# Optimization experiments

Measured on AMD Instinct MI355X. Metric: run time of the kernel, lower is better.

The kernel has to match this reference:

```python
import jax, jax.numpy as jnp
import numpy as np

B, N, C, H = 2, 2048, 512, 8
D = C // H  # head dim = 64
SCALE = C ** -0.5  # module uses heads_channels**-0.5 (full inner dim, not per-head)


def setup_inputs() -> dict:
    key = jax.random.key(0)
    ks = jax.random.split(key, 9)
    return {
        "q": jax.random.normal(ks[0], (B, N, C), jnp.float32),
        "kv": jax.random.normal(ks[1], (B, N, C), jnp.float32),
        "pos_q": jax.random.normal(ks[2], (B, N, D), jnp.float32),
        "pos_k": jax.random.normal(ks[3], (B, N, D), jnp.float32),
        "Wq": jax.random.normal(ks[4], (C, C), jnp.float32) * (C ** -0.5),
        "Wk": jax.random.normal(ks[5], (C, C), jnp.float32) * (C ** -0.5),
        "Wv": jax.random.normal(ks[6], (C, C), jnp.float32) * (C ** -0.5),
        "Wo": jax.random.normal(ks[7], (C, C), jnp.float32) * (C ** -0.5),
        "bo": jnp.zeros((C,), jnp.float32),
    }


def reference(q, kv, pos_q, pos_k, Wq, Wk, Wv, Wo, bo):
    # projections: [b n c] @ [c c] -> [b n c]
    qp = q @ Wq
    kp = kv @ Wk
    vp = kv @ Wv
    # split heads: b n (h d) -> b h n d
    split = lambda t: t.reshape(B, N, H, D).transpose(0, 2, 1, 3)
    qh, kh, vh = split(qp), split(kp), split(vp)
    # additive positional bias, broadcast over heads: b n d -> b 1 n d
    qh = qh + pos_q[:, None, :, :]
    kh = kh + pos_k[:, None, :, :]
    sim = jnp.einsum("bhid,bhjd->bhij", qh, kh) * SCALE
    attn = jax.nn.softmax(sim, axis=-1)
    out = jnp.einsum("bhij,bhjd->bhid", attn, vh)
    # merge heads: b h n d -> b n (h d)
    out = out.transpose(0, 2, 1, 3).reshape(B, N, C)
    return out @ Wo + bo
```

## Files before the change

### kernel.cpp

```cpp
#include <hip/hip_runtime.h>
#include <hip/hip_bf16.h>
#include <stdint.h>
#include <math.h>

static constexpr int kB = 2, kN = 2048, kC = 512, kH = 8, kD = 64;
static constexpr float kScaleL2E =
    (float)(0.044194173824159216 * 1.4426950408889634);
static constexpr float kShift = 12.0f;
static constexpr int kSplit = 4;
static constexpr size_t kSegF = (size_t)kB * kN * kC;

typedef short bf16x8 __attribute__((ext_vector_type(8)));
typedef short bf16x4 __attribute__((ext_vector_type(4)));
typedef float f32x4  __attribute__((ext_vector_type(4)));

__device__ __forceinline__ float bf2f(unsigned short u) {
  union { unsigned int i; float f; } v; v.i = ((unsigned int)u) << 16; return v.f;
}
__device__ __forceinline__ unsigned short f2bf(float f) {
  union { float f; unsigned int i; } v; v.f = f;
  unsigned int x = v.i;
  return (unsigned short)((x + 0x7FFFu + ((x >> 16) & 1u)) >> 16);
}
__device__ __forceinline__ short f2bs(float f) { return (short)f2bf(f); }
__device__ __forceinline__ unsigned int pack2_t(float lo, float hi) {
  union { float f; unsigned int i; } a, b; a.f = lo; b.f = hi;
  return (b.i & 0xFFFF0000u) | (a.i >> 16);
}

__global__ __launch_bounds__(256) void prep_kernel(
    const float* __restrict__ q, const float* __restrict__ kv,
    const float* __restrict__ Wq, const float* __restrict__ Wk,
    const float* __restrict__ Wv,
    unsigned short* __restrict__ qbf, unsigned short* __restrict__ kvbf,
    unsigned short* __restrict__ wT)
{
  const int t = threadIdx.x;
  if (blockIdx.z == 0) {
    const int gid = blockIdx.x * 256 + t;
    #pragma unroll
    for (int it = 0; it < 8; ++it) {
      int i4 = gid + it * 65536;
      float4 a = *(const float4*)(q + (size_t)i4 * 4);
      float4 b = *(const float4*)(kv + (size_t)i4 * 4);
      bf16x4 ab = {f2bs(a.x), f2bs(a.y), f2bs(a.z), f2bs(a.w)};
      bf16x4 bb = {f2bs(b.x), f2bs(b.y), f2bs(b.z), f2bs(b.w)};
      *(bf16x4*)(qbf + (size_t)i4 * 4) = ab;
      *(bf16x4*)(kvbf + (size_t)i4 * 4) = bb;
    }
  } else {
    if (blockIdx.x >= 192) return;
    const int wsel = blockIdx.x >> 6;
    const int tile = blockIdx.x & 63;
    const int tr = tile >> 3, tc = tile & 7;
    const float* W = (wsel == 0) ? Wq : (wsel == 1 ? Wk : Wv);
    unsigned short* out = wT + (size_t)wsel * kC * kC;

    __shared__ __align__(16) float Ts[64][68];
    #pragma unroll
    for (int it = 0; it < 4; ++it) {
      int e = t + it * 256;
      int r = e >> 4, c4 = (e & 15) * 4;
      *(float4*)&Ts[r][c4] =
          *(const float4*)(W + (size_t)(tr * 64 + r) * kC + tc * 64 + c4);
    }
    __syncthreads();
    const int n = t >> 2, ks = (t & 3) * 16;
    unsigned short* orow = out + (size_t)(tc * 64 + n) * kC + tr * 64 + ks;
    #pragma unroll
    for (int c = 0; c < 4; ++c) {
      ushort4 o;
      o.x = f2bf(Ts[ks + c * 4 + 0][n]);
      o.y = f2bf(Ts[ks + c * 4 + 1][n]);
      o.z = f2bf(Ts[ks + c * 4 + 2][n]);
      o.w = f2bf(Ts[ks + c * 4 + 3][n]);
      *(ushort4*)(orow + c * 4) = o;
    }
  }
}

__global__ __launch_bounds__(256) void proj_kernel(
    const unsigned short* __restrict__ qbf,
    const unsigned short* __restrict__ kvbf,
    const unsigned short* __restrict__ wT,
    const float* __restrict__ pos_q,
    const float* __restrict__ pos_k,
    unsigned short* __restrict__ qh,
    unsigned short* __restrict__ kh,
    unsigned short* __restrict__ vhT)
{
  const bool kvmode = (blockIdx.z == 1);
  const unsigned short* A = kvmode ? kvbf : qbf;
  const unsigned short* Bt0 = wT + (kvmode ? (size_t)kC * kC : 0);
  const unsigned short* Bt1 = wT + 2 * (size_t)kC * kC;

  __shared__ __align__(16) unsigned short As[128][72];
  __shared__ __align__(16) unsigned short Bs[2][64][72];

  const int t = threadIdx.x;
  const int w = t >> 6, lane = t & 63;
  const int l15 = lane & 15, quad = lane >> 4;
  const int m0 = blockIdx.x * 128;
  const int n0 = blockIdx.y * 64;

  const int sr = t >> 3, sc = (t & 7) * 8;

  bf16x8 pa[4], pb0[2], pb1[2];
  #pragma unroll
  for (int i = 0; i < 4; ++i)
    pa[i] = *(const bf16x8*)(A + (size_t)(m0 + sr + i * 32) * kC + sc);
  #pragma unroll
  for (int i = 0; i < 2; ++i)
    pb0[i] = *(const bf16x8*)(Bt0 + (size_t)(n0 + sr + i * 32) * kC + sc);
  if (kvmode)
    #pragma unroll
    for (int i = 0; i < 2; ++i)
      pb1[i] = *(const bf16x8*)(Bt1 + (size_t)(n0 + sr + i * 32) * kC + sc);

  f32x4 acc0[2][4], acc1[2][4];
  #pragma unroll
  for (int si = 0; si < 2; ++si)
    #pragma unroll
    for (int ct = 0; ct < 4; ++ct) {
      acc0[si][ct] = (f32x4){0.f, 0.f, 0.f, 0.f};
      acc1[si][ct] = (f32x4){0.f, 0.f, 0.f, 0.f};
    }

  for (int k0 = 0; k0 < kC; k0 += 64) {
    if (k0) __syncthreads();
    #pragma unroll
    for (int i = 0; i < 4; ++i) *(bf16x8*)&As[sr + i * 32][sc] = pa[i];
    #pragma unroll
    for (int i = 0; i < 2; ++i) *(bf16x8*)&Bs[0][sr + i * 32][sc] = pb0[i];
    if (kvmode)
      #pragma unroll
      for (int i = 0; i < 2; ++i) *(bf16x8*)&Bs[1][sr + i * 32][sc] = pb1[i];
    __syncthreads();
    if (k0 + 64 < kC) {
      int kn = k0 + 64;
      #pragma unroll
      for (int i = 0; i < 4; ++i)
        pa[i] = *(const bf16x8*)(A + (size_t)(m0 + sr + i * 32) * kC + kn + sc);
      #pragma unroll
      for (int i = 0; i < 2; ++i)
        pb0[i] = *(const bf16x8*)(Bt0 + (size_t)(n0 + sr + i * 32) * kC + kn + sc);
      if (kvmode)
        #pragma unroll
        for (int i = 0; i < 2; ++i)
          pb1[i] = *(const bf16x8*)(Bt1 + (size_t)(n0 + sr + i * 32) * kC + kn + sc);
    }
    bf16x8 a0[2], a1[2];
    #pragma unroll
    for (int si = 0; si < 2; ++si) {
      a0[si] = *(const bf16x8*)&As[w * 32 + si * 16 + l15][quad * 8];
      a1[si] = *(const bf16x8*)&As[w * 32 + si * 16 + l15][32 + quad * 8];
    }
    #pragma unroll
    for (int ct = 0; ct < 4; ++ct) {
      bf16x8 b0 = *(const bf16x8*)&Bs[0][ct * 16 + l15][quad * 8];
      bf16x8 b1 = *(const bf16x8*)&Bs[0][ct * 16 + l15][32 + quad * 8];
      #pragma unroll
      for (int si = 0; si < 2; ++si) {
        acc0[si][ct] = __builtin_amdgcn_mfma_f32_16x16x32_bf16(a0[si], b0, acc0[si][ct], 0, 0, 0);
        acc0[si][ct] = __builtin_amdgcn_mfma_f32_16x16x32_bf16(a1[si], b1, acc0[si][ct], 0, 0, 0);
      }
      if (kvmode) {
        bf16x8 c0 = *(const bf16x8*)&Bs[1][ct * 16 + l15][quad * 8];
        bf16x8 c1 = *(const bf16x8*)&Bs[1][ct * 16 + l15][32 + quad * 8];
        #pragma unroll
        for (int si = 0; si < 2; ++si) {
          acc1[si][ct] = __builtin_amdgcn_mfma_f32_16x16x32_bf16(a0[si], c0, acc1[si][ct], 0, 0, 0);
          acc1[si][ct] = __builtin_amdgcn_mfma_f32_16x16x32_bf16(a1[si], c1, acc1[si][ct], 0, 0, 0);
        }
      }
    }
  }

  const int h = n0 >> 6;
  #pragma unroll
  for (int si = 0; si < 2; ++si)
    #pragma unroll
    for (int r = 0; r < 4; ++r) {
      int m = m0 + w * 32 + si * 16 + quad * 4 + r;
      int b = m >> 11, n_seq = m & (kN - 1);
      #pragma unroll
      for (int ct = 0; ct < 4; ++ct) {
        int d = ct * 16 + l15;
        if (!kvmode) {
          float val = (acc0[si][ct][r] +
                       pos_q[((size_t)b * kN + n_seq) * kD + d]) * kScaleL2E;
          qh[(((size_t)b * kH + h) * kN + n_seq) * kD + d] = f2bf(val);
        } else {
          float vk = acc0[si][ct][r] + pos_k[((size_t)b * kN + n_seq) * kD + d];
          kh[(((size_t)b * kH + h) * kN + n_seq) * kD + d] = f2bf(vk);
          vhT[(((size_t)b * kH + h) * kD + d) * kN + n_seq] = f2bf(acc1[si][ct][r]);
        }
      }
    }
}

__global__ __launch_bounds__(256, 4) void attn_kernel(
    const unsigned short* __restrict__ qh,
    const unsigned short* __restrict__ kh,
    const unsigned short* __restrict__ vhT,
    unsigned short* __restrict__ opart,
    float* __restrict__ lbuf)
{
  const int bh = blockIdx.y;
  const int b = bh >> 3, h = bh & 7;
  const int q0 = blockIdx.x * 128;
  const int s = blockIdx.z;
  const int kbase = s * (kN / kSplit);
  const int nkt = kN / kSplit / 64;
  const int t = threadIdx.x;
  const int w = t >> 6, lane = t & 63;
  const int l15 = lane & 15, quad = lane >> 4;

  __shared__ __align__(16) unsigned short Kbf[2][64][72];
  __shared__ __align__(16) unsigned short Vt[2][64][72];

  const unsigned short* Qb = qh  + (size_t)bh * kN * kD;
  const unsigned short* Kb = kh  + (size_t)bh * kN * kD;
  const unsigned short* Vb = vhT + (size_t)bh * kD * kN;

  bf16x8 aq[2][2];
  #pragma unroll
  for (int g = 0; g < 2; ++g) {
    const unsigned short* qrow = Qb + (size_t)(q0 + w * 32 + g * 16 + l15) * kD;
    aq[g][0] = *(const bf16x8*)(qrow + quad * 8);
    aq[g][1] = *(const bf16x8*)(qrow + 32 + quad * 8);
  }

  const int sr = t >> 3, sc = (t & 7) * 8, sr2 = sr + 32;

  bf16x8 pk0 = *(const bf16x8*)(Kb + (size_t)(kbase + sr) * kD + sc);
  bf16x8 pk1 = *(const bf16x8*)(Kb + (size_t)(kbase + sr2) * kD + sc);
  bf16x8 pv0 = *(const bf16x8*)(Vb + (size_t)sr * kN + kbase + sc);
  bf16x8 pv1 = *(const bf16x8*)(Vb + (size_t)sr2 * kN + kbase + sc);
  *(bf16x8*)&Kbf[0][sr][sc]  = pk0;
  *(bf16x8*)&Kbf[0][sr2][sc] = pk1;
  *(bf16x8*)&Vt[0][sr][sc]   = pv0;
  *(bf16x8*)&Vt[0][sr2][sc]  = pv1;
  {
    int kt1 = kbase + 64;
    pk0 = *(const bf16x8*)(Kb + (size_t)(kt1 + sr) * kD + sc);
    pk1 = *(const bf16x8*)(Kb + (size_t)(kt1 + sr2) * kD + sc);
    pv0 = *(const bf16x8*)(Vb + (size_t)sr * kN + kt1 + sc);
    pv1 = *(const bf16x8*)(Vb + (size_t)sr2 * kN + kt1 + sc);
  }

  f32x4 o[2][4];
  #pragma unroll
  for (int g = 0; g < 2; ++g)
    #pragma unroll
    for (int nt = 0; nt < 4; ++nt) o[g][nt] = (f32x4){0.f, 0.f, 0.f, 0.f};
  float l_run[2] = {0.f, 0.f};

  const int src_a = l15 + 32 * (quad & 1);
  const int src_b = src_a + 16;
  const bool hi_sel = (quad & 2) != 0;

  for (int i = 0; i < nkt; ++i) {
    __syncthreads();
    if (i + 1 < nkt) {
      unsigned short (*Kw)[72] = Kbf[(i + 1) & 1];
      unsigned short (*Vw)[72] = Vt[(i + 1) & 1];
      *(bf16x8*)&Kw[sr][sc]  = pk0;
      *(bf16x8*)&Kw[sr2][sc] = pk1;
      *(bf16x8*)&Vw[sr][sc]  = pv0;
      *(bf16x8*)&Vw[sr2][sc] = pv1;
      if (i + 2 < nkt) {
        int ktn = kbase + (i + 2) * 64;
        pk0 = *(const bf16x8*)(Kb + (size_t)(ktn + sr) * kD + sc);
        pk1 = *(const bf16x8*)(Kb + (size_t)(ktn + sr2) * kD + sc);
        pv0 = *(const bf16x8*)(Vb + (size_t)sr * kN + ktn + sc);
        pv1 = *(const bf16x8*)(Vb + (size_t)sr2 * kN + ktn + sc);
      }
    }
    const unsigned short (*Kr)[72] = Kbf[i & 1];
    const unsigned short (*Vr)[72] = Vt[i & 1];

    f32x4 sacc[2][4];
    #pragma unroll
    for (int ct = 0; ct < 4; ++ct) {
      bf16x8 ak0 = *(const bf16x8*)&Kr[ct * 16 + l15][quad * 8];
      bf16x8 ak1 = *(const bf16x8*)&Kr[ct * 16 + l15][32 + quad * 8];
      #pragma unroll
      for (int g = 0; g < 2; ++g) {
        f32x4 zz = (f32x4){0.f, 0.f, 0.f, 0.f};
        zz = __builtin_amdgcn_mfma_f32_16x16x32_bf16(ak0, aq[g][0], zz, 0, 0, 0);
        zz = __builtin_amdgcn_mfma_f32_16x16x32_bf16(ak1, aq[g][1], zz, 0, 0, 0);
        sacc[g][ct] = zz;
      }
    }

    union PF { unsigned int u[4]; bf16x8 v; } pf[2][2];
    #pragma unroll
    for (int g = 0; g < 2; ++g) {
      float psum = 0.f;
      #pragma unroll
      for (int ct = 0; ct < 4; ++ct)
        #pragma unroll
        for (int r = 0; r < 4; ++r) {
          float p = exp2f(sacc[g][ct][r] - kShift);
          sacc[g][ct][r] = p;
          psum += p;
        }
      psum += __shfl_xor(psum, 16);
      psum += __shfl_xor(psum, 32);
      l_run[g] += psum;

      unsigned int pk01[4], pk23[4];
      #pragma unroll
      for (int ct = 0; ct < 4; ++ct) {
        pk01[ct] = pack2_t(sacc[g][ct][0], sacc[g][ct][1]);
        pk23[ct] = pack2_t(sacc[g][ct][2], sacc[g][ct][3]);
      }
      unsigned int s01a[4], s23a[4], s01b[4], s23b[4];
      #pragma unroll
      for (int ct = 0; ct < 4; ++ct) {
        s01a[ct] = (unsigned int)__shfl((int)pk01[ct], src_a);
        s23a[ct] = (unsigned int)__shfl((int)pk23[ct], src_a);
        s01b[ct] = (unsigned int)__shfl((int)pk01[ct], src_b);
        s23b[ct] = (unsigned int)__shfl((int)pk23[ct], src_b);
      }
      pf[g][0].u[0] = hi_sel ? s01a[1] : s01a[0];
      pf[g][0].u[1] = hi_sel ? s23a[1] : s23a[0];
      pf[g][0].u[2] = hi_sel ? s01b[1] : s01b[0];
      pf[g][0].u[3] = hi_sel ? s23b[1] : s23b[0];
      pf[g][1].u[0] = hi_sel ? s01a[3] : s01a[2];
      pf[g][1].u[1] = hi_sel ? s23a[3] : s23a[2];
      pf[g][1].u[2] = hi_sel ? s01b[3] : s01b[2];
      pf[g][1].u[3] = hi_sel ? s23b[3] : s23b[2];
    }

    #pragma unroll
    for (int nt = 0; nt < 4; ++nt) {
      bf16x8 av0 = *(const bf16x8*)&Vr[nt * 16 + l15][quad * 8];
      bf16x8 av1 = *(const bf16x8*)&Vr[nt * 16 + l15][32 + quad * 8];
      #pragma unroll
      for (int g = 0; g < 2; ++g) {
        o[g][nt] = __builtin_amdgcn_mfma_f32_16x16x32_bf16(av0, pf[g][0].v, o[g][nt], 0, 0, 0);
        o[g][nt] = __builtin_amdgcn_mfma_f32_16x16x32_bf16(av1, pf[g][1].v, o[g][nt], 0, 0, 0);
      }
    }
  }

  unsigned short* od = opart + (size_t)s * kSegF;
  #pragma unroll
  for (int g = 0; g < 2; ++g) {
    const int n = q0 + w * 32 + g * 16 + l15;
    unsigned short* obase = od + ((size_t)b * kN + n) * kC + h * kD + quad * 4;
    #pragma unroll
    for (int nt = 0; nt < 4; ++nt) {
      ushort4 st;
      st.x = f2bf(o[g][nt][0]);
      st.y = f2bf(o[g][nt][1]);
      st.z = f2bf(o[g][nt][2]);
      st.w = f2bf(o[g][nt][3]);
      *(ushort4*)(obase + nt * 16) = st;
    }
    if (quad == 0) lbuf[(size_t)(s * 16 + bh) * kN + n] = l_run[g];
  }
}

__global__ __launch_bounds__(256) void combine_kernel(
    const unsigned short* __restrict__ opart,
    const float* __restrict__ lbuf,
    unsigned short* __restrict__ ao)
{
  const size_t f = ((size_t)blockIdx.x * 256 + threadIdx.x) * 8;
  const int c = (int)(f & (kC - 1));
  const int n = (int)((f >> 9) & (kN - 1));
  const int b = (int)(f >> 20);
  const int bh = b * 8 + (c >> 6);
  float lsum = 0.f;
  #pragma unroll
  for (int s = 0; s < kSplit; ++s)
    lsum += lbuf[(size_t)(s * 16 + bh) * kN + n];
  float wgt = 1.f / lsum;
  float acc[8] = {};
  #pragma unroll
  for (int s = 0; s < kSplit; ++s) {
    bf16x8 v = *(const bf16x8*)(opart + (size_t)s * kSegF + f);
    #pragma unroll
    for (int j = 0; j < 8; ++j) acc[j] += bf2f((unsigned short)v[j]);
  }
  bf16x8 r;
  #pragma unroll
  for (int j = 0; j < 8; ++j) r[j] = (short)f2bf(acc[j] * wgt);
  *(bf16x8*)(ao + f) = r;
}

__global__ __launch_bounds__(256) void proj_out_kernel(
    const unsigned short* __restrict__ ao,
    const float* __restrict__ Wo,
    const float* __restrict__ bo,
    float* __restrict__ out)
{
  __shared__ __align__(16) unsigned short Wt[64][72];

  const int t = threadIdx.x;
  const int w = t >> 6, lane = t & 63;
  const int l15 = lane & 15, quad = lane >> 4;
  const int m0 = blockIdx.x * 64;
  const int n0 = blockIdx.y * 64;

  const unsigned short* arow = ao + (size_t)(m0 + w * 16 + l15) * kC;

  ushort4 pw[4];
  #pragma unroll
  for (int i = 0; i < 4; ++i) {
    int e = t + i * 256;
    int r = e >> 4, c4 = (e & 15) * 4;
    float4 wv = *(const float4*)(Wo + (size_t)r * kC + n0 + c4);
    pw[i] = make_ushort4(f2bf(wv.x), f2bf(wv.y), f2bf(wv.z), f2bf(wv.w));
  }
  bf16x8 pa0 = *(const bf16x8*)(arow + quad * 8);
  bf16x8 pa1 = *(const bf16x8*)(arow + 32 + quad * 8);

  f32x4 acc[4];
  #pragma unroll
  for (int ct = 0; ct < 4; ++ct) acc[ct] = (f32x4){0.f, 0.f, 0.f, 0.f};

  for (int k0 = 0; k0 < kC; k0 += 64) {
    if (k0) __syncthreads();
    #pragma unroll
    for (int i = 0; i < 4; ++i) {
      int e = t + i * 256;
      int r = e >> 4, c4 = (e & 15) * 4;
      Wt[c4 + 0][r] = pw[i].x;
      Wt[c4 + 1][r] = pw[i].y;
      Wt[c4 + 2][r] = pw[i].z;
      Wt[c4 + 3][r] = pw[i].w;
    }
    __syncthreads();
    bf16x8 a0 = pa0, a1 = pa1;
    if (k0 + 64 < kC) {
      int kn = k0 + 64;
      #pragma unroll
      for (int i = 0; i < 4; ++i) {
        int e = t + i * 256;
        int r = e >> 4, c4 = (e & 15) * 4;
        float4 wv = *(const float4*)(Wo + (size_t)(kn + r) * kC + n0 + c4);
        pw[i] = make_ushort4(f2bf(wv.x), f2bf(wv.y), f2bf(wv.z), f2bf(wv.w));
      }
      pa0 = *(const bf16x8*)(arow + kn + quad * 8);
      pa1 = *(const bf16x8*)(arow + kn + 32 + quad * 8);
    }
    #pragma unroll
    for (int ct = 0; ct < 4; ++ct) {
      bf16x8 b0 = *(const bf16x8*)&Wt[ct * 16 + l15][quad * 8];
      bf16x8 b1 = *(const bf16x8*)&Wt[ct * 16 + l15][32 + quad * 8];
      acc[ct] = __builtin_amdgcn_mfma_f32_16x16x32_bf16(a0, b0, acc[ct], 0, 0, 0);
      acc[ct] = __builtin_amdgcn_mfma_f32_16x16x32_bf16(a1, b1, acc[ct], 0, 0, 0);
    }
  }

  #pragma unroll
  for (int ct = 0; ct < 4; ++ct) {
    int n = n0 + ct * 16 + l15;
    float bb = bo[n];
    #pragma unroll
    for (int r = 0; r < 4; ++r) {
      int m = m0 + w * 16 + quad * 4 + r;
      out[(size_t)m * kC + n] = acc[ct][r] + bb;
    }
  }
}

extern "C" void kernel_launch(void* const* d_in, const int* in_sizes, int n_in,
                              void* d_out, int out_size, void* d_ws, size_t ws_size,
                              hipStream_t stream) {
  (void)in_sizes; (void)n_in; (void)out_size; (void)ws_size;
  const float* q     = (const float*)d_in[0];
  const float* kv    = (const float*)d_in[1];
  const float* pos_q = (const float*)d_in[2];
  const float* pos_k = (const float*)d_in[3];
  const float* Wq    = (const float*)d_in[4];
  const float* Wk    = (const float*)d_in[5];
  const float* Wv    = (const float*)d_in[6];
  const float* Wo    = (const float*)d_in[7];
  const float* bo    = (const float*)d_in[8];
  float* out = (float*)d_out;

  const size_t seg = (size_t)kB * kH * kN * kD;

  unsigned short* qbf  = (unsigned short*)d_ws;
  unsigned short* kvbf = qbf + seg;
  unsigned short* wT   = kvbf + seg;
  unsigned short* qhp  = wT + 3 * (size_t)kC * kC;
  unsigned short* khp  = qhp + seg;
  unsigned short* vtp  = khp + seg;
  unsigned short* opart = vtp + seg;
  float* lbuf = (float*)(opart + (size_t)kSplit * kSegF);
  unsigned short* aop = (unsigned short*)(lbuf + (size_t)kSplit * 16 * kN);

  dim3 blk(256);
  prep_kernel<<<dim3(256, 1, 2), blk, 0, stream>>>(q, kv, Wq, Wk, Wv, qbf, kvbf, wT);
  proj_kernel<<<dim3(32, 8, 2), blk, 0, stream>>>(qbf, kvbf, wT, pos_q, pos_k,
                                                  qhp, khp, vtp);
  attn_kernel<<<dim3(16, 16, kSplit), blk, 0, stream>>>(qhp, khp, vtp, opart, lbuf);
  combine_kernel<<<dim3(1024), blk, 0, stream>>>(opart, lbuf, aop);
  proj_out_kernel<<<dim3(64, 8), blk, 0, stream>>>(aop, Wo, bo, out);
}
```

Before: 163.7 us.

## Fuse fp32-to-bf16 conversion and weight transpose into projection GEMM

Removes the separate prep kernel that converted q/kv to bf16 and wrote transposed bf16 weights. The projection kernel now loads fp32 activations and weights directly, converts them while staging into shared memory, and transposes the weights with scalar LDS stores. This saves a launch and a round trip of the intermediate bf16 buffers. In exchange it drops the register prefetch pipelining, reads twice as many bytes per tile, repeats the conversion in every block, and adds scattered 2-byte LDS stores that may conflict on banks.

```diff
diff --git a/kernel.cpp b/kernel.cpp
--- a/kernel.cpp
+++ b/kernel.cpp
@@ -28,61 +28,12 @@
   return (b.i & 0xFFFF0000u) | (a.i >> 16);
 }
 
-__global__ __launch_bounds__(256) void prep_kernel(
-    const float* __restrict__ q, const float* __restrict__ kv,
-    const float* __restrict__ Wq, const float* __restrict__ Wk,
+__global__ __launch_bounds__(256) void proj_kernel(
+    const float* __restrict__ q,
+    const float* __restrict__ kv,
+    const float* __restrict__ Wq,
+    const float* __restrict__ Wk,
     const float* __restrict__ Wv,
-    unsigned short* __restrict__ qbf, unsigned short* __restrict__ kvbf,
-    unsigned short* __restrict__ wT)
-{
-  const int t = threadIdx.x;
-  if (blockIdx.z == 0) {
-    const int gid = blockIdx.x * 256 + t;
-    #pragma unroll
-    for (int it = 0; it < 8; ++it) {
-      int i4 = gid + it * 65536;
-      float4 a = *(const float4*)(q + (size_t)i4 * 4);
-      float4 b = *(const float4*)(kv + (size_t)i4 * 4);
-      bf16x4 ab = {f2bs(a.x), f2bs(a.y), f2bs(a.z), f2bs(a.w)};
-      bf16x4 bb = {f2bs(b.x), f2bs(b.y), f2bs(b.z), f2bs(b.w)};
-      *(bf16x4*)(qbf + (size_t)i4 * 4) = ab;
-      *(bf16x4*)(kvbf + (size_t)i4 * 4) = bb;
-    }
-  } else {
-    if (blockIdx.x >= 192) return;
-    const int wsel = blockIdx.x >> 6;
-    const int tile = blockIdx.x & 63;
-    const int tr = tile >> 3, tc = tile & 7;
-    const float* W = (wsel == 0) ? Wq : (wsel == 1 ? Wk : Wv);
-    unsigned short* out = wT + (size_t)wsel * kC * kC;
-
-    __shared__ __align__(16) float Ts[64][68];
-    #pragma unroll
-    for (int it = 0; it < 4; ++it) {
-      int e = t + it * 256;
-      int r = e >> 4, c4 = (e & 15) * 4;
-      *(float4*)&Ts[r][c4] =
-          *(const float4*)(W + (size_t)(tr * 64 + r) * kC + tc * 64 + c4);
-    }
-    __syncthreads();
-    const int n = t >> 2, ks = (t & 3) * 16;
-    unsigned short* orow = out + (size_t)(tc * 64 + n) * kC + tr * 64 + ks;
-    #pragma unroll
-    for (int c = 0; c < 4; ++c) {
-      ushort4 o;
-      o.x = f2bf(Ts[ks + c * 4 + 0][n]);
-      o.y = f2bf(Ts[ks + c * 4 + 1][n]);
-      o.z = f2bf(Ts[ks + c * 4 + 2][n]);
-      o.w = f2bf(Ts[ks + c * 4 + 3][n]);
-      *(ushort4*)(orow + c * 4) = o;
-    }
-  }
-}
-
-__global__ __launch_bounds__(256) void proj_kernel(
-    const unsigned short* __restrict__ qbf,
-    const unsigned short* __restrict__ kvbf,
-    const unsigned short* __restrict__ wT,
     const float* __restrict__ pos_q,
     const float* __restrict__ pos_k,
     unsigned short* __restrict__ qh,
@@ -90,9 +41,9 @@
     unsigned short* __restrict__ vhT)
 {
   const bool kvmode = (blockIdx.z == 1);
-  const unsigned short* A = kvmode ? kvbf : qbf;
-  const unsigned short* Bt0 = wT + (kvmode ? (size_t)kC * kC : 0);
-  const unsigned short* Bt1 = wT + 2 * (size_t)kC * kC;
+  const float* A  = kvmode ? kv : q;
+  const float* W0 = kvmode ? Wk : Wq;
+  const float* W1 = Wv;
 
   __shared__ __align__(16) unsigned short As[128][72];
   __shared__ __align__(16) unsigned short Bs[2][64][72];
@@ -103,20 +54,6 @@
   const int m0 = blockIdx.x * 128;
   const int n0 = blockIdx.y * 64;
 
-  const int sr = t >> 3, sc = (t & 7) * 8;
-
-  bf16x8 pa[4], pb0[2], pb1[2];
-  #pragma unroll
-  for (int i = 0; i < 4; ++i)
-    pa[i] = *(const bf16x8*)(A + (size_t)(m0 + sr + i * 32) * kC + sc);
-  #pragma unroll
-  for (int i = 0; i < 2; ++i)
-    pb0[i] = *(const bf16x8*)(Bt0 + (size_t)(n0 + sr + i * 32) * kC + sc);
-  if (kvmode)
-    #pragma unroll
-    for (int i = 0; i < 2; ++i)
-      pb1[i] = *(const bf16x8*)(Bt1 + (size_t)(n0 + sr + i * 32) * kC + sc);
-
   f32x4 acc0[2][4], acc1[2][4];
   #pragma unroll
   for (int si = 0; si < 2; ++si)
@@ -127,28 +64,39 @@
     }
 
   for (int k0 = 0; k0 < kC; k0 += 64) {
-    if (k0) __syncthreads();
-    #pragma unroll
-    for (int i = 0; i < 4; ++i) *(bf16x8*)&As[sr + i * 32][sc] = pa[i];
-    #pragma unroll
-    for (int i = 0; i < 2; ++i) *(bf16x8*)&Bs[0][sr + i * 32][sc] = pb0[i];
-    if (kvmode)
-      #pragma unroll
-      for (int i = 0; i < 2; ++i) *(bf16x8*)&Bs[1][sr + i * 32][sc] = pb1[i];
     __syncthreads();
-    if (k0 + 64 < kC) {
-      int kn = k0 + 64;
-      #pragma unroll
-      for (int i = 0; i < 4; ++i)
-        pa[i] = *(const bf16x8*)(A + (size_t)(m0 + sr + i * 32) * kC + kn + sc);
-      #pragma unroll
-      for (int i = 0; i < 2; ++i)
-        pb0[i] = *(const bf16x8*)(Bt0 + (size_t)(n0 + sr + i * 32) * kC + kn + sc);
-      if (kvmode)
-        #pragma unroll
-        for (int i = 0; i < 2; ++i)
-          pb1[i] = *(const bf16x8*)(Bt1 + (size_t)(n0 + sr + i * 32) * kC + kn + sc);
-    }
+    #pragma unroll
+    for (int i = 0; i < 8; ++i) {
+      int e = t + i * 256;
+      int r = e >> 4, c4 = (e & 15) * 4;
+      float4 av = *(const float4*)(A + (size_t)(m0 + r) * kC + k0 + c4);
+      bf16x4 ab = {f2bs(av.x), f2bs(av.y), f2bs(av.z), f2bs(av.w)};
+      *(bf16x4*)&As[r][c4] = ab;
+    }
+    #pragma unroll
+    for (int i = 0; i < 4; ++i) {
+      int e = t + i * 256;
+      int r = e >> 4, c4 = (e & 15) * 4;
+      float4 wv = *(const float4*)(W0 + (size_t)(k0 + r) * kC + n0 + c4);
+      Bs[0][c4 + 0][r] = f2bf(wv.x);
+      Bs[0][c4 + 1][r] = f2bf(wv.y);
+      Bs[0][c4 + 2][r] = f2bf(wv.z);
+      Bs[0][c4 + 3][r] = f2bf(wv.w);
+    }
+    if (kvmode) {
+      #pragma unroll
+      for (int i = 0; i < 4; ++i) {
+        int e = t + i * 256;
+        int r = e >> 4, c4 = (e & 15) * 4;
+        float4 wv = *(const float4*)(W1 + (size_t)(k0 + r) * kC + n0 + c4);
+        Bs[1][c4 + 0][r] = f2bf(wv.x);
+        Bs[1][c4 + 1][r] = f2bf(wv.y);
+        Bs[1][c4 + 2][r] = f2bf(wv.z);
+        Bs[1][c4 + 3][r] = f2bf(wv.w);
+      }
+    }
+    __syncthreads();
+
     bf16x8 a0[2], a1[2];
     #pragma unroll
     for (int si = 0; si < 2; ++si) {
@@ -486,10 +434,7 @@
 
   const size_t seg = (size_t)kB * kH * kN * kD;
 
-  unsigned short* qbf  = (unsigned short*)d_ws;
-  unsigned short* kvbf = qbf + seg;
-  unsigned short* wT   = kvbf + seg;
-  unsigned short* qhp  = wT + 3 * (size_t)kC * kC;
+  unsigned short* qhp  = (unsigned short*)d_ws;
   unsigned short* khp  = qhp + seg;
   unsigned short* vtp  = khp + seg;
   unsigned short* opart = vtp + seg;
@@ -497,8 +442,7 @@
   unsigned short* aop = (unsigned short*)(lbuf + (size_t)kSplit * 16 * kN);
 
   dim3 blk(256);
-  prep_kernel<<<dim3(256, 1, 2), blk, 0, stream>>>(q, kv, Wq, Wk, Wv, qbf, kvbf, wT);
-  proj_kernel<<<dim3(32, 8, 2), blk, 0, stream>>>(qbf, kvbf, wT, pos_q, pos_k,
+  proj_kernel<<<dim3(32, 8, 2), blk, 0, stream>>>(q, kv, Wq, Wk, Wv, pos_q, pos_k,
                                                   qhp, khp, vtp);
   attn_kernel<<<dim3(16, 16, kSplit), blk, 0, stream>>>(qhp, khp, vtp, opart, lbuf);
   combine_kernel<<<dim3(1024), blk, 0, stream>>>(opart, lbuf, aop);
```

Result: slower. 192.3 us (+17.5%).
